# Kernel optimization log

Hardware: AMD Instinct MI355X
Metric: run time of the kernel (lower is better)

Reference implementation:

```python
import jax, jax.numpy as jnp
import numpy as np

N_NODES = 100000
N_EDGES = 600000
D_FEAT = 128
N_CLASSES = 64


def setup_inputs() -> dict:
    key = jax.random.key(0)
    k_h, k_src, k_dst, k_w = jax.random.split(key, 4)
    h = jax.random.normal(k_h, (N_NODES, D_FEAT), dtype=jnp.float32)
    src = jax.random.randint(k_src, (N_EDGES,), 0, N_NODES, dtype=jnp.int64)
    dst = jax.random.randint(k_dst, (N_EDGES,), 0, N_NODES, dtype=jnp.int64)
    # nn.Linear(2*D_FEAT, N_CLASSES): weight [out, in], bias [out]
    W = jax.random.normal(k_w, (N_CLASSES, 2 * D_FEAT), dtype=jnp.float32) * (1.0 / np.sqrt(2 * D_FEAT))
    b = jnp.zeros((N_CLASSES,), dtype=jnp.float32)
    return {"h": h, "src": src, "dst": dst, "W": W, "b": b}


def reference(h, src, dst, W, b):
    # score = Linear(concat([h[src], h[dst]], -1))
    # Split W to avoid materializing the [n_edges, 2*d] concat:
    # concat @ W.T == h[src] @ W[:, :d].T + h[dst] @ W[:, d:].T
    d = h.shape[1]
    Wu = W[:, :d]  # [out, d]
    Wv = W[:, d:]  # [out, d]
    score = (jnp.einsum('ed,cd->ec', h[src], Wu)
             + jnp.einsum('ed,cd->ec', h[dst], Wv)
             + b)
    return score  # [n_edges, out_classes]
```

## Files before the change

kernel.cpp:

```cpp
#include <hip/hip_runtime.h>

#define N_NODES   100000
#define N_EDGES   600000
#define D_FEAT    128
#define N_CLASSES 64

typedef short bf16x8 __attribute__((ext_vector_type(8)));
typedef float f32x4  __attribute__((ext_vector_type(4)));
typedef unsigned short u16x8 __attribute__((ext_vector_type(8)));

__device__ __forceinline__ unsigned short f2bf(float f) {
    unsigned int u = __float_as_uint(f);
    unsigned int r = (u + 0x7fffu + ((u >> 16) & 1u)) >> 16;
    return (unsigned short)r;
}
__device__ __forceinline__ float bf2f(unsigned short u) {
    return __uint_as_float((unsigned int)u << 16);
}

__global__ __launch_bounds__(256) void proj_mfma(const float* __restrict__ h,
                                                 const float* __restrict__ W,
                                                 const float* __restrict__ b,
                                                 unsigned short* __restrict__ P) {
    __shared__ unsigned short WcS[128 * 128];

    const int wave = (blockIdx.x * 256 + threadIdx.x) >> 6;
    const int lane = threadIdx.x & 63;
    const int n0   = wave * 16;
    const bool valid = (n0 < N_NODES);
    const int m    = lane & 15;
    const int quad = lane >> 4;

    bf16x8 hfrag[4];
    if (valid) {
        const float* hrow = h + (size_t)(n0 + m) * 128 + quad * 8;
#pragma unroll
        for (int ks = 0; ks < 4; ++ks) {
            f32x4 v0 = __builtin_nontemporal_load((const f32x4*)(hrow + ks * 32));
            f32x4 v1 = __builtin_nontemporal_load((const f32x4*)(hrow + ks * 32 + 4));
            bf16x8 a;
            a[0] = (short)f2bf(v0[0]); a[1] = (short)f2bf(v0[1]);
            a[2] = (short)f2bf(v0[2]); a[3] = (short)f2bf(v0[3]);
            a[4] = (short)f2bf(v1[0]); a[5] = (short)f2bf(v1[1]);
            a[6] = (short)f2bf(v1[2]); a[7] = (short)f2bf(v1[3]);
            hfrag[ks] = a;
        }
    }

    {
        const int t = threadIdx.x;
#pragma unroll
        for (int i = 0; i < 16; ++i) {
            int cc = i * 256 + t;
            int c  = cc >> 5;
            int kc = (cc & 31) << 2;
            const float* wp = (c < 64) ? (W + c * 256 + kc)
                                       : (W + (c - 64) * 256 + 128 + kc);
            f32x4 v = *(const f32x4*)wp;
            ushort4 pk;
            pk.x = f2bf(v[0]); pk.y = f2bf(v[1]);
            pk.z = f2bf(v[2]); pk.w = f2bf(v[3]);
            int phys = (((kc >> 3) ^ (c & 15)) << 3) | (kc & 7);
            *(ushort4*)(WcS + c * 128 + phys) = pk;
        }
    }
    __syncthreads();
    if (!valid) return;

    f32x4 acc[8];
#pragma unroll
    for (int ct = 0; ct < 8; ++ct) acc[ct] = (f32x4){0.f, 0.f, 0.f, 0.f};

#pragma unroll
    for (int ct = 0; ct < 8; ++ct) {
        const unsigned short* wbase = WcS + (ct * 16 + m) * 128;
#pragma unroll
        for (int ks = 0; ks < 4; ++ks) {
            bf16x8 wfrag = *(const bf16x8*)(wbase + (((ks * 4 + quad) ^ m) << 3));
            acc[ct] = __builtin_amdgcn_mfma_f32_16x16x32_bf16(wfrag, hfrag[ks], acc[ct], 0, 0, 0);
        }
    }

    const int node = n0 + m;
    unsigned short* prow = P + (size_t)node * 128;
#pragma unroll
    for (int ct = 0; ct < 8; ++ct) {
        const int cb = ct * 16 + quad * 4;
        float v[4];
        if (cb < 64) {
            f32x4 bb = *(const f32x4*)(b + cb);
#pragma unroll
            for (int r = 0; r < 4; ++r) v[r] = acc[ct][r] + bb[r];
        } else {
#pragma unroll
            for (int r = 0; r < 4; ++r) v[r] = acc[ct][r];
        }
        ushort4 pk;
        pk.x = f2bf(v[0]); pk.y = f2bf(v[1]);
        pk.z = f2bf(v[2]); pk.w = f2bf(v[3]);
        *(ushort4*)(prow + cb) = pk;
    }
}

__global__ __launch_bounds__(256) void edge_kernel(const int* __restrict__ src,
                                                   const int* __restrict__ dst,
                                                   const unsigned short* __restrict__ P,
                                                   float* __restrict__ out) {
    int g  = blockIdx.x * 256 + threadIdx.x;
    int e0 = g >> 3;
    int c0 = (g & 7) << 3;
    int e1 = e0 + (N_EDGES / 2);
    int s0 = src[e0], d0 = dst[e0];
    int s1 = src[e1], d1 = dst[e1];
    u16x8 us0 = *(const u16x8*)(P + (size_t)s0 * 128 + c0);
    u16x8 ud0 = *(const u16x8*)(P + (size_t)d0 * 128 + 64 + c0);
    u16x8 us1 = *(const u16x8*)(P + (size_t)s1 * 128 + c0);
    u16x8 ud1 = *(const u16x8*)(P + (size_t)d1 * 128 + 64 + c0);

    f32x4 a0, a1, b0, b1;
#pragma unroll
    for (int j = 0; j < 4; ++j) {
        a0[j] = bf2f(us0[j])     + bf2f(ud0[j]);
        a1[j] = bf2f(us0[j + 4]) + bf2f(ud0[j + 4]);
        b0[j] = bf2f(us1[j])     + bf2f(ud1[j]);
        b1[j] = bf2f(us1[j + 4]) + bf2f(ud1[j + 4]);
    }
    float* op0 = out + (size_t)e0 * 64 + c0;
    float* op1 = out + (size_t)e1 * 64 + c0;
    __builtin_nontemporal_store(a0, (f32x4*)op0);
    __builtin_nontemporal_store(a1, (f32x4*)(op0 + 4));
    __builtin_nontemporal_store(b0, (f32x4*)op1);
    __builtin_nontemporal_store(b1, (f32x4*)(op1 + 4));
}

__global__ __launch_bounds__(256) void direct_kernel(const float* __restrict__ h,
                                                     const int* __restrict__ src,
                                                     const int* __restrict__ dst,
                                                     const float* __restrict__ W,
                                                     const float* __restrict__ b,
                                                     float* __restrict__ out) {
    __shared__ float hcat[4][256];
    int t = threadIdx.x;
    int w = t >> 6, lane = t & 63;
    int e = blockIdx.x * 4 + w;
    bool valid = (e < N_EDGES);
    if (valid) {
        int s = src[e], d = dst[e];
        const float* p = (lane < 32) ? (h + (size_t)s * 128 + lane * 4)
                                     : (h + (size_t)d * 128 + (lane - 32) * 4);
        *(float4*)&hcat[w][lane * 4] = *(const float4*)p;
    }
    __syncthreads();
    if (!valid) return;
    int c = lane;
    float acc = 0.f;
    for (int k = 0; k < 256; k += 4) {
        float4 wv = *(const float4*)(W + c * 256 + k);
        acc += hcat[w][k] * wv.x + hcat[w][k + 1] * wv.y
             + hcat[w][k + 2] * wv.z + hcat[w][k + 3] * wv.w;
    }
    out[(size_t)e * 64 + c] = acc + b[c];
}

extern "C" void kernel_launch(void* const* d_in, const int* in_sizes, int n_in,
                              void* d_out, int out_size, void* d_ws, size_t ws_size,
                              hipStream_t stream) {
    const float* h   = (const float*)d_in[0];
    const int*   src = (const int*)d_in[1];
    const int*   dst = (const int*)d_in[2];
    const float* W   = (const float*)d_in[3];
    const float* b   = (const float*)d_in[4];
    float* out = (float*)d_out;

    const size_t p_bytes = (size_t)N_NODES * 128 * sizeof(unsigned short);
    if (ws_size >= p_bytes) {
        unsigned short* P = (unsigned short*)d_ws;
        const int n_waves  = N_NODES / 16;
        const int n_blocks = (n_waves + 3) / 4;
        proj_mfma<<<n_blocks, 256, 0, stream>>>(h, W, b, P);
        edge_kernel<<<(N_EDGES / 2 * 8) / 256, 256, 0, stream>>>(src, dst, P, out);
    } else {
        direct_kernel<<<(N_EDGES + 3) / 4, 256, 0, stream>>>(h, src, dst, W, b, out);
    }
}
```

Before: 234.4 us.

## Fuse projection and edge gather into one cooperative persistent kernel with grid sync

Replaces the two-kernel projection-then-gather sequence with one persistent cooperative kernel of 512 blocks. The blocks first compute node projections in grid-stride tiles, then sync the whole grid and run the edge gather-add loop. This removes a kernel launch boundary and amortizes the W-to-LDS bf16 conversion across many tiles per block instead of once per small block. It also makes the projection stores nontemporal. The cost is fewer blocks for the latency-bound gather phase and grid-sync overhead, and the old two-kernel path stays as a fallback if the cooperative launch fails.

```diff
diff --git a/kernel.cpp b/kernel.cpp
--- a/kernel.cpp
+++ b/kernel.cpp
@@ -1,13 +1,19 @@
 #include <hip/hip_runtime.h>
+#include <hip/hip_cooperative_groups.h>
+
+namespace cg = cooperative_groups;
 
 #define N_NODES   100000
 #define N_EDGES   600000
 #define D_FEAT    128
 #define N_CLASSES 64
+#define N_TILES   (N_NODES / 16)
+#define GRID_BLKS 512
 
 typedef short bf16x8 __attribute__((ext_vector_type(8)));
 typedef float f32x4  __attribute__((ext_vector_type(4)));
 typedef unsigned short u16x8 __attribute__((ext_vector_type(8)));
+typedef unsigned short u16x4 __attribute__((ext_vector_type(4)));
 
 __device__ __forceinline__ unsigned short f2bf(float f) {
     unsigned int u = __float_as_uint(f);
@@ -18,54 +24,43 @@
     return __uint_as_float((unsigned int)u << 16);
 }
 
-__global__ __launch_bounds__(256) void proj_mfma(const float* __restrict__ h,
-                                                 const float* __restrict__ W,
-                                                 const float* __restrict__ b,
-                                                 unsigned short* __restrict__ P) {
-    __shared__ unsigned short WcS[128 * 128];
-
-    const int wave = (blockIdx.x * 256 + threadIdx.x) >> 6;
-    const int lane = threadIdx.x & 63;
-    const int n0   = wave * 16;
-    const bool valid = (n0 < N_NODES);
-    const int m    = lane & 15;
-    const int quad = lane >> 4;
-
+__device__ __forceinline__ void build_wc_lds(unsigned short* WcS,
+                                             const float* __restrict__ W,
+                                             int t) {
+#pragma unroll
+    for (int i = 0; i < 16; ++i) {
+        int cc = i * 256 + t;
+        int c  = cc >> 5;
+        int kc = (cc & 31) << 2;
+        const float* wp = (c < 64) ? (W + c * 256 + kc)
+                                   : (W + (c - 64) * 256 + 128 + kc);
+        f32x4 v = *(const f32x4*)wp;
+        u16x4 pk;
+        pk[0] = f2bf(v[0]); pk[1] = f2bf(v[1]);
+        pk[2] = f2bf(v[2]); pk[3] = f2bf(v[3]);
+        int phys = (((kc >> 3) ^ (c & 15)) << 3) | (kc & 7);
+        *(u16x4*)(WcS + c * 128 + phys) = pk;
+    }
+}
+
+__device__ __forceinline__ void proj_tile(const unsigned short* WcS,
+                                          const float* __restrict__ h,
+                                          const f32x4* bias,
+                                          unsigned short* __restrict__ P,
+                                          int n0, int m, int quad) {
     bf16x8 hfrag[4];
-    if (valid) {
-        const float* hrow = h + (size_t)(n0 + m) * 128 + quad * 8;
-#pragma unroll
-        for (int ks = 0; ks < 4; ++ks) {
-            f32x4 v0 = __builtin_nontemporal_load((const f32x4*)(hrow + ks * 32));
-            f32x4 v1 = __builtin_nontemporal_load((const f32x4*)(hrow + ks * 32 + 4));
-            bf16x8 a;
-            a[0] = (short)f2bf(v0[0]); a[1] = (short)f2bf(v0[1]);
-            a[2] = (short)f2bf(v0[2]); a[3] = (short)f2bf(v0[3]);
-            a[4] = (short)f2bf(v1[0]); a[5] = (short)f2bf(v1[1]);
-            a[6] = (short)f2bf(v1[2]); a[7] = (short)f2bf(v1[3]);
-            hfrag[ks] = a;
-        }
-    }
-
-    {
-        const int t = threadIdx.x;
-#pragma unroll
-        for (int i = 0; i < 16; ++i) {
-            int cc = i * 256 + t;
-            int c  = cc >> 5;
-            int kc = (cc & 31) << 2;
-            const float* wp = (c < 64) ? (W + c * 256 + kc)
-                                       : (W + (c - 64) * 256 + 128 + kc);
-            f32x4 v = *(const f32x4*)wp;
-            ushort4 pk;
-            pk.x = f2bf(v[0]); pk.y = f2bf(v[1]);
-            pk.z = f2bf(v[2]); pk.w = f2bf(v[3]);
-            int phys = (((kc >> 3) ^ (c & 15)) << 3) | (kc & 7);
-            *(ushort4*)(WcS + c * 128 + phys) = pk;
-        }
-    }
-    __syncthreads();
-    if (!valid) return;
+    const float* hrow = h + (size_t)(n0 + m) * 128 + quad * 8;
+#pragma unroll
+    for (int ks = 0; ks < 4; ++ks) {
+        f32x4 v0 = __builtin_nontemporal_load((const f32x4*)(hrow + ks * 32));
+        f32x4 v1 = __builtin_nontemporal_load((const f32x4*)(hrow + ks * 32 + 4));
+        bf16x8 a;
+        a[0] = (short)f2bf(v0[0]); a[1] = (short)f2bf(v0[1]);
+        a[2] = (short)f2bf(v0[2]); a[3] = (short)f2bf(v0[3]);
+        a[4] = (short)f2bf(v1[0]); a[5] = (short)f2bf(v1[1]);
+        a[6] = (short)f2bf(v1[2]); a[7] = (short)f2bf(v1[3]);
+        hfrag[ks] = a;
+    }
 
     f32x4 acc[8];
 #pragma unroll
@@ -81,32 +76,30 @@
         }
     }
 
-    const int node = n0 + m;
-    unsigned short* prow = P + (size_t)node * 128;
+    unsigned short* prow = P + (size_t)(n0 + m) * 128;
 #pragma unroll
     for (int ct = 0; ct < 8; ++ct) {
         const int cb = ct * 16 + quad * 4;
         float v[4];
-        if (cb < 64) {
-            f32x4 bb = *(const f32x4*)(b + cb);
-#pragma unroll
-            for (int r = 0; r < 4; ++r) v[r] = acc[ct][r] + bb[r];
+        if (ct < 4) {
+#pragma unroll
+            for (int r = 0; r < 4; ++r) v[r] = acc[ct][r] + bias[ct][r];
         } else {
 #pragma unroll
             for (int r = 0; r < 4; ++r) v[r] = acc[ct][r];
         }
-        ushort4 pk;
-        pk.x = f2bf(v[0]); pk.y = f2bf(v[1]);
-        pk.z = f2bf(v[2]); pk.w = f2bf(v[3]);
-        *(ushort4*)(prow + cb) = pk;
-    }
-}
-
-__global__ __launch_bounds__(256) void edge_kernel(const int* __restrict__ src,
-                                                   const int* __restrict__ dst,
-                                                   const unsigned short* __restrict__ P,
-                                                   float* __restrict__ out) {
-    int g  = blockIdx.x * 256 + threadIdx.x;
+        u16x4 pk;
+        pk[0] = f2bf(v[0]); pk[1] = f2bf(v[1]);
+        pk[2] = f2bf(v[2]); pk[3] = f2bf(v[3]);
+        __builtin_nontemporal_store(pk, (u16x4*)(prow + cb));
+    }
+}
+
+__device__ __forceinline__ void edge_item(int g,
+                                          const int* __restrict__ src,
+                                          const int* __restrict__ dst,
+                                          const unsigned short* __restrict__ P,
+                                          float* __restrict__ out) {
     int e0 = g >> 3;
     int c0 = (g & 7) << 3;
     int e1 = e0 + (N_EDGES / 2);
@@ -131,6 +124,75 @@
     __builtin_nontemporal_store(a1, (f32x4*)(op0 + 4));
     __builtin_nontemporal_store(b0, (f32x4*)op1);
     __builtin_nontemporal_store(b1, (f32x4*)(op1 + 4));
+}
+
+__global__ __launch_bounds__(256, 2) void fused_kernel(
+        const float* __restrict__ h,
+        const float* __restrict__ W,
+        const float* __restrict__ b,
+        unsigned short* __restrict__ P,
+        const int* __restrict__ src,
+        const int* __restrict__ dst,
+        float* __restrict__ out) {
+    __shared__ unsigned short WcS[128 * 128];
+
+    const int t    = threadIdx.x;
+    const int lane = t & 63;
+    const int wid  = t >> 6;
+    const int m    = lane & 15;
+    const int quad = lane >> 4;
+
+    build_wc_lds(WcS, W, t);
+    __syncthreads();
+
+    f32x4 bias[4];
+#pragma unroll
+    for (int ct = 0; ct < 4; ++ct)
+        bias[ct] = *(const f32x4*)(b + ct * 16 + quad * 4);
+
+    for (int tile = blockIdx.x * 4 + wid; tile < N_TILES; tile += gridDim.x * 4)
+        proj_tile(WcS, h, bias, P, tile * 16, m, quad);
+
+    __threadfence();
+    cg::this_grid().sync();
+
+    const int total  = (N_EDGES / 2) * 8;
+    const int stride = gridDim.x * 256;
+    for (int g = blockIdx.x * 256 + t; g < total; g += stride)
+        edge_item(g, src, dst, P, out);
+}
+
+__global__ __launch_bounds__(256) void proj_mfma(const float* __restrict__ h,
+                                                 const float* __restrict__ W,
+                                                 const float* __restrict__ b,
+                                                 unsigned short* __restrict__ P) {
+    __shared__ unsigned short WcS[128 * 128];
+    const int t    = threadIdx.x;
+    const int lane = t & 63;
+    const int wid  = t >> 6;
+    const int m    = lane & 15;
+    const int quad = lane >> 4;
+
+    build_wc_lds(WcS, W, t);
+    __syncthreads();
+
+    const int tile = blockIdx.x * 4 + wid;
+    if (tile >= N_TILES) return;
+
+    f32x4 bias[4];
+#pragma unroll
+    for (int ct = 0; ct < 4; ++ct)
+        bias[ct] = *(const f32x4*)(b + ct * 16 + quad * 4);
+
+    proj_tile(WcS, h, bias, P, tile * 16, m, quad);
+}
+
+__global__ __launch_bounds__(256) void edge_kernel(const int* __restrict__ src,
+                                                   const int* __restrict__ dst,
+                                                   const unsigned short* __restrict__ P,
+                                                   float* __restrict__ out) {
+    int g = blockIdx.x * 256 + threadIdx.x;
+    edge_item(g, src, dst, P, out);
 }
 
 __global__ __launch_bounds__(256) void direct_kernel(const float* __restrict__ h,
@@ -175,10 +237,22 @@
     const size_t p_bytes = (size_t)N_NODES * 128 * sizeof(unsigned short);
     if (ws_size >= p_bytes) {
         unsigned short* P = (unsigned short*)d_ws;
-        const int n_waves  = N_NODES / 16;
-        const int n_blocks = (n_waves + 3) / 4;
-        proj_mfma<<<n_blocks, 256, 0, stream>>>(h, W, b, P);
-        edge_kernel<<<(N_EDGES / 2 * 8) / 256, 256, 0, stream>>>(src, dst, P, out);
+        static int coop_ok = -1;
+        bool launched = false;
+        if (coop_ok != 0) {
+            void* args[] = {(void*)&h, (void*)&W, (void*)&b, (void*)&P,
+                            (void*)&src, (void*)&dst, (void*)&out};
+            hipError_t e = hipLaunchCooperativeKernel((const void*)fused_kernel,
+                                                      dim3(GRID_BLKS), dim3(256),
+                                                      args, 0, stream);
+            if (e == hipSuccess) { coop_ok = 1; launched = true; }
+            else                 { coop_ok = 0; }
+        }
+        if (!launched) {
+            const int n_blocks = (N_TILES + 3) / 4;
+            proj_mfma<<<n_blocks, 256, 0, stream>>>(h, W, b, P);
+            edge_kernel<<<(N_EDGES / 2 * 8) / 256, 256, 0, stream>>>(src, dst, P, out);
+        }
     } else {
         direct_kernel<<<(N_EDGES + 3) / 4, 256, 0, stream>>>(h, src, dst, W, b, out);
     }
```

After: 238.1 us. Within noise of the previous version (+1.6%).
